# Kernel optimization log

Hardware: AMD Instinct MI355X
Metric: run time of the kernel (lower is better)

## Reference

```python
import jax, jax.numpy as jnp
import numpy as np

M = 4  # num_modals
EPS = 1e-6


def setup_inputs() -> dict:
    key = jax.random.key(0)
    ks = jax.random.split(key, 12)
    c, h, r, B, n = 768, 3072, 16, 4, 1024
    inp = {
        "x": jax.random.normal(ks[0], (M * B, n, c), jnp.float32),
        "fc1_w": jax.random.normal(ks[1], (h, c), jnp.float32) * 0.02,
        "fc1_b": jax.random.normal(ks[2], (h,), jnp.float32) * 0.02,
        "fc2_w": jax.random.normal(ks[3], (c, h), jnp.float32) * 0.02,
        "fc2_b": jax.random.normal(ks[4], (c,), jnp.float32) * 0.02,
        "a_fc1": jax.random.normal(ks[5], (M, r, c), jnp.float32) * 0.02,
        "b_fc1": jax.random.normal(ks[6], (M, h, r), jnp.float32) * 0.02,
        "a_fc2": jax.random.normal(ks[7], (M, r, h), jnp.float32) * 0.02,
        "b_fc2": jax.random.normal(ks[8], (M, c, r), jnp.float32) * 0.02,
        "gate_w": jax.random.normal(ks[9], (M, M, c), jnp.float32) * 0.02,
        "gate_b": jax.random.normal(ks[10], (M, M), jnp.float32) * 0.02,
        "modality_mask": jax.random.randint(ks[11], (M, B), 0, 2, jnp.int32),
    }
    return inp


def _fused_combine(rw, mask_f, lora):
    # rw: [M,B,n,M] routing softmax; mask_f: [M,B]; lora: [M,B,n,d]
    # per_routing_weights[i,j,t,k] = rw[i,j,t,k] * mask[k,j], renormalized over k
    masked = rw * mask_f.T[None, :, None, :]                      # [M,B,n,M]
    norm = masked / (jnp.sum(masked, axis=-1, keepdims=True) + EPS)
    fused = jnp.einsum("ibnk,kbnd->ibnd", norm, lora)             # combine experts
    return fused * mask_f[:, :, None, None]                       # rows with mask==0 stay zero


def reference(x, fc1_w, fc1_b, fc2_w, fc2_b, a_fc1, b_fc1, a_fc2, b_fc2,
              gate_w, gate_b, modality_mask):
    bs_m, n, c = x.shape
    B = bs_m // M
    xm = x.reshape(M, B, n, c)
    mask_f = modality_mask.astype(x.dtype)                        # [M,B]

    # base fc1
    x1 = (jnp.einsum("ibnc,hc->ibnh", xm, fc1_w) + fc1_b)         # [M,B,n,h]

    # per-modality routing softmax over M experts (computed in fp32 as in torch)
    logits = jnp.einsum("ibnc,iec->ibne", xm, gate_w) + gate_b[:, None, None, :]
    rw = jax.nn.softmax(logits.astype(jnp.float32), axis=-1).astype(x.dtype)

    # HiRA delta for fc1: elementwise(fc1_w, B@A) per modality
    delta1 = fc1_w[None] * jnp.einsum("ihr,irc->ihc", b_fc1, a_fc1)  # [M,h,c]
    lora1 = jnp.einsum("ibnc,ihc->ibnh", xm, delta1)              # [M,B,n,h]

    x1 = x1 + _fused_combine(rw, mask_f, lora1)
    x1 = jax.nn.gelu(x1, approximate=False)                       # mlp.act

    # base fc2
    x2 = jnp.einsum("ibnh,ch->ibnc", x1, fc2_w) + fc2_b           # [M,B,n,c]

    # HiRA delta for fc2
    delta2 = fc2_w[None] * jnp.einsum("icr,irh->ich", b_fc2, a_fc2)  # [M,c,h]
    lora2 = jnp.einsum("ibnh,ich->ibnc", x1, delta2)              # [M,B,n,c]

    x2 = x2 + _fused_combine(rw, mask_f, lora2)
    return x2.reshape(bs_m, n, c)
```

## Files before the change

### kernel.cpp

```cpp
#include <hip/hip_runtime.h>
#include <hip/hip_bf16.h>
#include <math.h>

#define NMOD 4
#define NB 4
#define NTOKN 1024
#define CDIM 768
#define HDIM 3072
#define RDIM 16
#define MROWS (NMOD*NB*NTOKN)
#define RPM (NB*NTOKN)

typedef __bf16 bf16_t;
typedef __bf16 bf16x4 __attribute__((ext_vector_type(4)));
typedef __bf16 bf16x8 __attribute__((ext_vector_type(8)));
typedef float f32x4 __attribute__((ext_vector_type(4)));

__global__ void cvt_kernel(const float* __restrict__ in, bf16_t* __restrict__ out, int n) {
  int i = (blockIdx.x * blockDim.x + threadIdx.x) * 4;
  if (i >= n) return;
  const float4 v = *reinterpret_cast<const float4*>(in + i);
  bf16x4 o;
  o[0] = (bf16_t)v.x; o[1] = (bf16_t)v.y; o[2] = (bf16_t)v.z; o[3] = (bf16_t)v.w;
  *reinterpret_cast<bf16x4*>(out + i) = o;
}

__global__ void delta1_kernel(const float* __restrict__ fc1w, const float* __restrict__ a1,
                              const float* __restrict__ b1, bf16_t* __restrict__ out) {
  int idx = blockIdx.x * blockDim.x + threadIdx.x;
  if (idx >= NMOD*HDIM*CDIM) return;
  int c = idx % CDIM;
  int h = (idx / CDIM) % HDIM;
  int k = idx / (CDIM*HDIM);
  const float* brow = b1 + ((size_t)k*HDIM + h)*RDIM;
  const float* acol = a1 + (size_t)k*RDIM*CDIM + c;
  float s = 0.f;
  #pragma unroll
  for (int r = 0; r < RDIM; ++r) s += brow[r] * acol[r*CDIM];
  out[idx] = (bf16_t)(fc1w[h*CDIM + c] * s);
}

__global__ void delta2_kernel(const float* __restrict__ fc2w, const float* __restrict__ a2,
                              const float* __restrict__ b2, bf16_t* __restrict__ out) {
  int idx = blockIdx.x * blockDim.x + threadIdx.x;
  if (idx >= NMOD*CDIM*HDIM) return;
  int h = idx % HDIM;
  int c = (idx / HDIM) % CDIM;
  int k = idx / (HDIM*CDIM);
  const float* brow = b2 + ((size_t)k*CDIM + c)*RDIM;
  const float* acol = a2 + (size_t)k*RDIM*HDIM + h;
  float s = 0.f;
  #pragma unroll
  for (int r = 0; r < RDIM; ++r) s += brow[r] * acol[r*HDIM];
  out[idx] = (bf16_t)(fc2w[c*HDIM + h] * s);
}

__global__ void gate_kernel(const float* __restrict__ x, const float* __restrict__ gw,
                            const float* __restrict__ gb, const int* __restrict__ mask,
                            float* __restrict__ normw, bf16_t* __restrict__ x_bf) {
  int t = blockIdx.x * 4 + (threadIdx.x >> 6);
  int lane = threadIdx.x & 63;
  int i = t >> 12;
  int b = (t >> 10) & 3;
  const float* xr = x + (size_t)t * CDIM;
  bf16_t* xo = x_bf + (size_t)t * CDIM;
  float acc[NMOD] = {0.f, 0.f, 0.f, 0.f};
  for (int c = lane; c < CDIM; c += 64) {
    float xv = xr[c];
    xo[c] = (bf16_t)xv;
    #pragma unroll
    for (int e = 0; e < NMOD; ++e) acc[e] += xv * gw[(i*NMOD + e)*CDIM + c];
  }
  #pragma unroll
  for (int e = 0; e < NMOD; ++e) {
    float v = acc[e];
    #pragma unroll
    for (int off = 32; off > 0; off >>= 1) v += __shfl_xor(v, off);
    acc[e] = v;
  }
  if (lane == 0) {
    float lg[NMOD], mx = -1e30f;
    #pragma unroll
    for (int e = 0; e < NMOD; ++e) { lg[e] = acc[e] + gb[i*NMOD + e]; mx = fmaxf(mx, lg[e]); }
    float s = 0.f;
    #pragma unroll
    for (int e = 0; e < NMOD; ++e) { lg[e] = expf(lg[e] - mx); s += lg[e]; }
    float inv = 1.f / s;
    float num[NMOD], den = 0.f;
    #pragma unroll
    for (int k = 0; k < NMOD; ++k) {
      float mk = (float)mask[k*NB + b];
      num[k] = lg[k] * inv * mk;
      den += num[k];
    }
    float mi = (float)mask[i*NB + b];
    float scale = mi / (den + 1e-6f);
    #pragma unroll
    for (int k = 0; k < NMOD; ++k) normw[(size_t)t*4 + k] = num[k] * scale;
  }
}

#define BMT 128
#define BNT 128
#define BKT 64

__device__ __forceinline__ void gload_lds16(const bf16_t* g, bf16_t* l) {
  __builtin_amdgcn_global_load_lds((const __attribute__((address_space(1))) void*)g,
                                   (__attribute__((address_space(3))) void*)l, 16, 0, 0);
}
#define MFMA_BF16 __builtin_amdgcn_mfma_f32_16x16x32_bf16

__global__ __launch_bounds__(256, 4)
void gemm_kernel(const bf16_t* __restrict__ A, const bf16_t* __restrict__ W0,
                 const bf16_t* __restrict__ WL, const float* __restrict__ bias,
                 const int* __restrict__ mask,
                 bf16_t* __restrict__ outB, bf16_t* __restrict__ outL,
                 int K, int N, int P, int modStride, int rowOff, int posOff) {
  __shared__ __align__(16) bf16_t As[BMT * BKT];
  __shared__ __align__(16) bf16_t Bs[BNT * BKT];

  const int tid  = threadIdx.x;
  const int lane = tid & 63;
  const int wv   = tid >> 6;
  const int wr   = wv >> 1, wc = wv & 1;
  const int row0 = blockIdx.x * BMT;
  const int col0 = blockIdx.y * BNT;
  const bool lora = (blockIdx.z != 0);

  const int mod = row0 / P;
  if (lora) {
    const int bb = (posOff + (row0 % P)) >> 10;
    if (mask[mod*NB + bb] == 0) return;
  }
  const int gArow0 = mod * modStride + rowOff + (row0 % P);
  const bf16_t* Wp = lora ? (WL + (size_t)mod * N * K) : W0;

  const int ldr = tid >> 3;
  const int ssl = ((tid & 7) ^ (ldr & 7)) * 8;
  const bf16_t* Ag = A  + (size_t)(gArow0 + ldr) * K + ssl;
  const bf16_t* Wg = Wp + (size_t)(col0   + ldr) * K + ssl;

  const int fr  = lane & 15;
  const int hi  = lane >> 4;
  const int sk0 = ((hi)     ^ (fr & 7)) * 8;
  const int sk1 = ((4 + hi) ^ (fr & 7)) * 8;

  f32x4 acc[4][4];
  #pragma unroll
  for (int i = 0; i < 4; ++i)
    #pragma unroll
    for (int j = 0; j < 4; ++j) acc[i][j] = (f32x4){0.f, 0.f, 0.f, 0.f};

  for (int k0 = 0; k0 < K; k0 += BKT) {
    __syncthreads();
    #pragma unroll
    for (int j = 0; j < 4; ++j)
      gload_lds16(Ag + (size_t)(j*32) * K + k0, &As[tid*8 + j*2048]);
    #pragma unroll
    for (int j = 0; j < 4; ++j)
      gload_lds16(Wg + (size_t)(j*32) * K + k0, &Bs[tid*8 + j*2048]);
    __syncthreads();

    #pragma unroll
    for (int kk = 0; kk < 2; ++kk) {
      const int sk = (kk == 0) ? sk0 : sk1;
      bf16x8 af[4], bfr[4];
      #pragma unroll
      for (int mi = 0; mi < 4; ++mi)
        af[mi] = *reinterpret_cast<const bf16x8*>(&As[(wr*64 + mi*16 + fr)*BKT + sk]);
      #pragma unroll
      for (int ni = 0; ni < 4; ++ni)
        bfr[ni] = *reinterpret_cast<const bf16x8*>(&Bs[(wc*64 + ni*16 + fr)*BKT + sk]);
      #pragma unroll
      for (int mi = 0; mi < 4; ++mi)
        #pragma unroll
        for (int ni = 0; ni < 4; ++ni)
          acc[mi][ni] = MFMA_BF16(af[mi], bfr[ni], acc[mi][ni], 0, 0, 0);
    }
  }

  bf16_t* outp = lora ? outL : outB;
  #pragma unroll
  for (int mi = 0; mi < 4; ++mi) {
    #pragma unroll
    for (int ni = 0; ni < 4; ++ni) {
      const int colg = col0 + wc*64 + ni*16 + fr;
      float bv = 0.f;
      if (!lora) bv = bias[colg];
      #pragma unroll
      for (int rg = 0; rg < 4; ++rg) {
        const int rowg = row0 + wr*64 + mi*16 + hi*4 + rg;
        outp[(size_t)rowg * N + colg] = (bf16_t)(acc[mi][ni][rg] + bv);
      }
    }
  }
}

__global__ void combine1_kernel(bf16_t* __restrict__ base1, const bf16_t* __restrict__ L1,
                                const float* __restrict__ normw, const int* __restrict__ mask,
                                int P, int chunkOff) {
  int idx = blockIdx.x * blockDim.x + threadIdx.x;
  if (idx >= P * (HDIM/8)) return;
  int h0 = (idx % (HDIM/8)) * 8;
  int p  = idx / (HDIM/8);
  const int b = (chunkOff + p) >> 10;
  float lv[4][8];
  #pragma unroll
  for (int k = 0; k < 4; ++k) {
    if (mask[k*NB + b] != 0) {
      bf16x8 v = *reinterpret_cast<const bf16x8*>(&L1[((size_t)(k*P + p))*HDIM + h0]);
      #pragma unroll
      for (int j = 0; j < 8; ++j) lv[k][j] = (float)v[j];
    } else {
      #pragma unroll
      for (int j = 0; j < 8; ++j) lv[k][j] = 0.f;
    }
  }
  #pragma unroll
  for (int i = 0; i < 4; ++i) {
    size_t ro = ((size_t)(i*P + p))*HDIM + h0;
    const float* nw = normw + ((size_t)(i*RPM + chunkOff + p))*4;
    float n0 = nw[0], n1 = nw[1], n2 = nw[2], n3 = nw[3];
    bf16x8 bv = *reinterpret_cast<const bf16x8*>(&base1[ro]);
    bf16x8 ov;
    #pragma unroll
    for (int j = 0; j < 8; ++j) {
      float v = (float)bv[j] + n0*lv[0][j] + n1*lv[1][j] + n2*lv[2][j] + n3*lv[3][j];
      float g = 0.5f * v * (1.f + erff(v * 0.70710678118654752f));
      ov[j] = (bf16_t)g;
    }
    *reinterpret_cast<bf16x8*>(&base1[ro]) = ov;
  }
}

__global__ void combine2_kernel(const bf16_t* __restrict__ base2, const bf16_t* __restrict__ L2,
                                const float* __restrict__ normw, const int* __restrict__ mask,
                                float* __restrict__ out, int P, int chunkOff) {
  int idx = blockIdx.x * blockDim.x + threadIdx.x;
  if (idx >= P * (CDIM/8)) return;
  int c0 = (idx % (CDIM/8)) * 8;
  int p  = idx / (CDIM/8);
  const int b = (chunkOff + p) >> 10;
  float lv[4][8];
  #pragma unroll
  for (int k = 0; k < 4; ++k) {
    if (mask[k*NB + b] != 0) {
      bf16x8 v = *reinterpret_cast<const bf16x8*>(&L2[((size_t)(k*P + p))*CDIM + c0]);
      #pragma unroll
      for (int j = 0; j < 8; ++j) lv[k][j] = (float)v[j];
    } else {
      #pragma unroll
      for (int j = 0; j < 8; ++j) lv[k][j] = 0.f;
    }
  }
  #pragma unroll
  for (int i = 0; i < 4; ++i) {
    int grow = i*RPM + chunkOff + p;
    const float* nw = normw + (size_t)grow*4;
    float n0 = nw[0], n1 = nw[1], n2 = nw[2], n3 = nw[3];
    bf16x8 bv = *reinterpret_cast<const bf16x8*>(&base2[((size_t)(i*P + p))*CDIM + c0]);
    float o[8];
    #pragma unroll
    for (int j = 0; j < 8; ++j)
      o[j] = (float)bv[j] + n0*lv[0][j] + n1*lv[1][j] + n2*lv[2][j] + n3*lv[3][j];
    float4* op = reinterpret_cast<float4*>(out + (size_t)grow*CDIM + c0);
    op[0] = make_float4(o[0], o[1], o[2], o[3]);
    op[1] = make_float4(o[4], o[5], o[6], o[7]);
  }
}

extern "C" void kernel_launch(void* const* d_in, const int* in_sizes, int n_in,
                              void* d_out, int out_size, void* d_ws, size_t ws_size,
                              hipStream_t stream) {
  (void)in_sizes; (void)n_in; (void)out_size;
  const float* x    = (const float*)d_in[0];
  const float* fc1w = (const float*)d_in[1];
  const float* fc1b = (const float*)d_in[2];
  const float* fc2w = (const float*)d_in[3];
  const float* fc2b = (const float*)d_in[4];
  const float* a1   = (const float*)d_in[5];
  const float* b1   = (const float*)d_in[6];
  const float* a2   = (const float*)d_in[7];
  const float* b2   = (const float*)d_in[8];
  const float* gw   = (const float*)d_in[9];
  const float* gb   = (const float*)d_in[10];
  const int*   mask = (const int*)d_in[11];
  float* out = (float*)d_out;

  char* ws = (char*)d_ws;
  size_t off = 0;
  auto carve = [&](size_t bytes) -> char* {
    char* p = ws + off; off += (bytes + 255) & ~(size_t)255; return p;
  };
  bf16_t* x_bf  = (bf16_t*)carve((size_t)MROWS*CDIM*2);
  bf16_t* w1_bf = (bf16_t*)carve((size_t)HDIM*CDIM*2);
  bf16_t* w2_bf = (bf16_t*)carve((size_t)CDIM*HDIM*2);
  bf16_t* d1_bf = (bf16_t*)carve((size_t)NMOD*HDIM*CDIM*2);
  bf16_t* d2_bf = (bf16_t*)carve((size_t)NMOD*CDIM*HDIM*2);
  float*  normw = (float*)carve((size_t)MROWS*4*4);
  const size_t fixedBytes = off;

  int P = RPM;
  while (P > 128 && fixedBytes + (size_t)61440*P + 4096 > ws_size) P >>= 1;
  const int NCH = RPM / P;

  bf16_t* base1 = (bf16_t*)carve((size_t)NMOD*P*HDIM*2);
  bf16_t* L1    = (bf16_t*)carve((size_t)NMOD*P*HDIM*2);
  bf16_t* base2 = (bf16_t*)carve((size_t)NMOD*P*CDIM*2);
  bf16_t* L2    = (bf16_t*)carve((size_t)NMOD*P*CDIM*2);

  cvt_kernel<<<HDIM*CDIM/1024, 256, 0, stream>>>(fc1w, w1_bf, HDIM*CDIM);
  cvt_kernel<<<CDIM*HDIM/1024, 256, 0, stream>>>(fc2w, w2_bf, CDIM*HDIM);
  delta1_kernel<<<NMOD*HDIM*CDIM/256, 256, 0, stream>>>(fc1w, a1, b1, d1_bf);
  delta2_kernel<<<NMOD*CDIM*HDIM/256, 256, 0, stream>>>(fc2w, a2, b2, d2_bf);
  gate_kernel<<<MROWS/4, 256, 0, stream>>>(x, gw, gb, mask, normw, x_bf);

  for (int g = 0; g < NCH; ++g) {
    const int chunkOff = g * P;
    gemm_kernel<<<dim3(NMOD*P/BMT, HDIM/BNT, 2), 256, 0, stream>>>(
        x_bf, w1_bf, d1_bf, fc1b, mask, base1, L1, CDIM, HDIM, P, RPM, chunkOff, chunkOff);
    combine1_kernel<<<(P*(HDIM/8) + 255)/256, 256, 0, stream>>>(base1, L1, normw, mask, P, chunkOff);
    gemm_kernel<<<dim3(NMOD*P/BMT, CDIM/BNT, 2), 256, 0, stream>>>(
        base1, w2_bf, d2_bf, fc2b, mask, base2, L2, HDIM, CDIM, P, P, 0, chunkOff);
    combine2_kernel<<<(P*(CDIM/8) + 255)/256, 256, 0, stream>>>(base2, L2, normw, mask, out, P, chunkOff);
  }
}
```

Before: 454.2 us.

## Prefetch next K tile during MFMA, fuse weight casts, alias scratch buffers

The GEMM main loop now loads all fragments for a tile into registers, then issues async global-to-LDS loads for the next tile before running the MFMAs, so memory latency overlaps compute. Launch bounds drop to 3 waves per SIMD to leave room for the extra registers. The separate fp32-to-bf16 weight cast kernels are folded into the delta kernels, which removes two launches and one re-read of the weights. Scratch buffers for L1, base2 and L2 are aliased to shrink the workspace, which may allow larger chunks. The single-buffered LDS with two barriers per iteration limits how much overlap is possible, and the lower occupancy is a risk.

```diff
diff --git a/kernel.cpp b/kernel.cpp
--- a/kernel.cpp
+++ b/kernel.cpp
@@ -12,21 +12,12 @@
 #define RPM (NB*NTOKN)
 
 typedef __bf16 bf16_t;
-typedef __bf16 bf16x4 __attribute__((ext_vector_type(4)));
 typedef __bf16 bf16x8 __attribute__((ext_vector_type(8)));
 typedef float f32x4 __attribute__((ext_vector_type(4)));
 
-__global__ void cvt_kernel(const float* __restrict__ in, bf16_t* __restrict__ out, int n) {
-  int i = (blockIdx.x * blockDim.x + threadIdx.x) * 4;
-  if (i >= n) return;
-  const float4 v = *reinterpret_cast<const float4*>(in + i);
-  bf16x4 o;
-  o[0] = (bf16_t)v.x; o[1] = (bf16_t)v.y; o[2] = (bf16_t)v.z; o[3] = (bf16_t)v.w;
-  *reinterpret_cast<bf16x4*>(out + i) = o;
-}
-
 __global__ void delta1_kernel(const float* __restrict__ fc1w, const float* __restrict__ a1,
-                              const float* __restrict__ b1, bf16_t* __restrict__ out) {
+                              const float* __restrict__ b1, bf16_t* __restrict__ out,
+                              bf16_t* __restrict__ w_bf) {
   int idx = blockIdx.x * blockDim.x + threadIdx.x;
   if (idx >= NMOD*HDIM*CDIM) return;
   int c = idx % CDIM;
@@ -37,11 +28,14 @@
   float s = 0.f;
   #pragma unroll
   for (int r = 0; r < RDIM; ++r) s += brow[r] * acol[r*CDIM];
-  out[idx] = (bf16_t)(fc1w[h*CDIM + c] * s);
+  const float wv = fc1w[h*CDIM + c];
+  out[idx] = (bf16_t)(wv * s);
+  if (k == 0) w_bf[h*CDIM + c] = (bf16_t)wv;
 }
 
 __global__ void delta2_kernel(const float* __restrict__ fc2w, const float* __restrict__ a2,
-                              const float* __restrict__ b2, bf16_t* __restrict__ out) {
+                              const float* __restrict__ b2, bf16_t* __restrict__ out,
+                              bf16_t* __restrict__ w_bf) {
   int idx = blockIdx.x * blockDim.x + threadIdx.x;
   if (idx >= NMOD*CDIM*HDIM) return;
   int h = idx % HDIM;
@@ -52,7 +46,9 @@
   float s = 0.f;
   #pragma unroll
   for (int r = 0; r < RDIM; ++r) s += brow[r] * acol[r*HDIM];
-  out[idx] = (bf16_t)(fc2w[c*HDIM + h] * s);
+  const float wv = fc2w[c*HDIM + h];
+  out[idx] = (bf16_t)(wv * s);
+  if (k == 0) w_bf[c*HDIM + h] = (bf16_t)wv;
 }
 
 __global__ void gate_kernel(const float* __restrict__ x, const float* __restrict__ gw,
@@ -110,7 +106,7 @@
 }
 #define MFMA_BF16 __builtin_amdgcn_mfma_f32_16x16x32_bf16
 
-__global__ __launch_bounds__(256, 4)
+__global__ __launch_bounds__(256, 3)
 void gemm_kernel(const bf16_t* __restrict__ A, const bf16_t* __restrict__ W0,
                  const bf16_t* __restrict__ WL, const float* __restrict__ bias,
                  const int* __restrict__ mask,
@@ -140,6 +136,15 @@
   const bf16_t* Ag = A  + (size_t)(gArow0 + ldr) * K + ssl;
   const bf16_t* Wg = Wp + (size_t)(col0   + ldr) * K + ssl;
 
+#define STAGE(k0_) do {                                                      \
+    _Pragma("unroll")                                                        \
+    for (int j_ = 0; j_ < 4; ++j_)                                           \
+      gload_lds16(Ag + (size_t)(j_*32)*K + (k0_), &As[tid*8 + j_*2048]);     \
+    _Pragma("unroll")                                                        \
+    for (int j_ = 0; j_ < 4; ++j_)                                           \
+      gload_lds16(Wg + (size_t)(j_*32)*K + (k0_), &Bs[tid*8 + j_*2048]);     \
+  } while (0)
+
   const int fr  = lane & 15;
   const int hi  = lane >> 4;
   const int sk0 = ((hi)     ^ (fr & 7)) * 8;
@@ -151,33 +156,39 @@
     #pragma unroll
     for (int j = 0; j < 4; ++j) acc[i][j] = (f32x4){0.f, 0.f, 0.f, 0.f};
 
-  for (int k0 = 0; k0 < K; k0 += BKT) {
+  const int NT = K / BKT;
+
+  STAGE(0);
+  __syncthreads();
+
+  for (int t = 0; t < NT; ++t) {
+    bf16x8 af[2][4], bfr[2][4];
+    #pragma unroll
+    for (int mi = 0; mi < 4; ++mi) {
+      af[0][mi] = *reinterpret_cast<const bf16x8*>(&As[(wr*64 + mi*16 + fr)*BKT + sk0]);
+      af[1][mi] = *reinterpret_cast<const bf16x8*>(&As[(wr*64 + mi*16 + fr)*BKT + sk1]);
+    }
+    #pragma unroll
+    for (int ni = 0; ni < 4; ++ni) {
+      bfr[0][ni] = *reinterpret_cast<const bf16x8*>(&Bs[(wc*64 + ni*16 + fr)*BKT + sk0]);
+      bfr[1][ni] = *reinterpret_cast<const bf16x8*>(&Bs[(wc*64 + ni*16 + fr)*BKT + sk1]);
+    }
     __syncthreads();
-    #pragma unroll
-    for (int j = 0; j < 4; ++j)
-      gload_lds16(Ag + (size_t)(j*32) * K + k0, &As[tid*8 + j*2048]);
-    #pragma unroll
-    for (int j = 0; j < 4; ++j)
-      gload_lds16(Wg + (size_t)(j*32) * K + k0, &Bs[tid*8 + j*2048]);
-    __syncthreads();
-
-    #pragma unroll
-    for (int kk = 0; kk < 2; ++kk) {
-      const int sk = (kk == 0) ? sk0 : sk1;
-      bf16x8 af[4], bfr[4];
-      #pragma unroll
-      for (int mi = 0; mi < 4; ++mi)
-        af[mi] = *reinterpret_cast<const bf16x8*>(&As[(wr*64 + mi*16 + fr)*BKT + sk]);
-      #pragma unroll
-      for (int ni = 0; ni < 4; ++ni)
-        bfr[ni] = *reinterpret_cast<const bf16x8*>(&Bs[(wc*64 + ni*16 + fr)*BKT + sk]);
+
+    if (t + 1 < NT) STAGE((t + 1) * BKT);
+    __builtin_amdgcn_sched_barrier(0);
+
+    #pragma unroll
+    for (int kk = 0; kk < 2; ++kk)
       #pragma unroll
       for (int mi = 0; mi < 4; ++mi)
         #pragma unroll
         for (int ni = 0; ni < 4; ++ni)
-          acc[mi][ni] = MFMA_BF16(af[mi], bfr[ni], acc[mi][ni], 0, 0, 0);
-    }
-  }
+          acc[mi][ni] = MFMA_BF16(af[kk][mi], bfr[kk][ni], acc[mi][ni], 0, 0, 0);
+
+    __syncthreads();
+  }
+#undef STAGE
 
   bf16_t* outp = lora ? outL : outB;
   #pragma unroll
@@ -301,18 +312,17 @@
   const size_t fixedBytes = off;
 
   int P = RPM;
-  while (P > 128 && fixedBytes + (size_t)61440*P + 4096 > ws_size) P >>= 1;
+  while (P > 128 && fixedBytes + (size_t)49152*P + 4096 > ws_size) P >>= 1;
   const int NCH = RPM / P;
 
   bf16_t* base1 = (bf16_t*)carve((size_t)NMOD*P*HDIM*2);
-  bf16_t* L1    = (bf16_t*)carve((size_t)NMOD*P*HDIM*2);
-  bf16_t* base2 = (bf16_t*)carve((size_t)NMOD*P*CDIM*2);
-  bf16_t* L2    = (bf16_t*)carve((size_t)NMOD*P*CDIM*2);
-
-  cvt_kernel<<<HDIM*CDIM/1024, 256, 0, stream>>>(fc1w, w1_bf, HDIM*CDIM);
-  cvt_kernel<<<CDIM*HDIM/1024, 256, 0, stream>>>(fc2w, w2_bf, CDIM*HDIM);
-  delta1_kernel<<<NMOD*HDIM*CDIM/256, 256, 0, stream>>>(fc1w, a1, b1, d1_bf);
-  delta2_kernel<<<NMOD*CDIM*HDIM/256, 256, 0, stream>>>(fc2w, a2, b2, d2_bf);
+  bf16_t* Lbuf  = (bf16_t*)carve((size_t)NMOD*P*HDIM*2);
+  bf16_t* L1    = Lbuf;
+  bf16_t* base2 = Lbuf;
+  bf16_t* L2    = Lbuf + (size_t)NMOD*P*CDIM;
+
+  delta1_kernel<<<NMOD*HDIM*CDIM/256, 256, 0, stream>>>(fc1w, a1, b1, d1_bf, w1_bf);
+  delta2_kernel<<<NMOD*CDIM*HDIM/256, 256, 0, stream>>>(fc2w, a2, b2, d2_bf, w2_bf);
   gate_kernel<<<MROWS/4, 256, 0, stream>>>(x, gw, gb, mask, normw, x_bf);
 
   for (int g = 0; g < NCH; ++g) {
```

Result: no change. 452.8 us (-0.3%).
